# Kernel optimization log

Measured on AMD Instinct MI355X. Metric: run time of the kernel, lower is better.

Reference implementation:

```python
import jax, jax.numpy as jnp
import numpy as np

N_SAMPLES = 131072
N_FEATURES = 64
N_TREES = 64
DEPTH = 12                      # complete binary trees
N_INTERNAL = 2 ** DEPTH - 1     # 4095 internal nodes per tree
N_LEAVES = 2 ** DEPTH           # 4096 leaves per tree
N_CLASSES = 8


def setup_inputs() -> dict:
    key = jax.random.key(0)
    k1, k2, k3, k4 = jax.random.split(key, 4)
    X = jax.random.normal(k1, (N_SAMPLES, N_FEATURES), dtype=jnp.float32)
    # flattened complete-binary-tree parameters (FIL-style layout)
    features = jax.random.randint(k2, (N_TREES, N_INTERNAL), 0, N_FEATURES, dtype=jnp.int32)
    thresholds = jax.random.normal(k3, (N_TREES, N_INTERNAL), dtype=jnp.float32)
    leaf_values = jax.random.randint(k4, (N_TREES, N_LEAVES), 0, N_CLASSES, dtype=jnp.int32)
    return {"X": X, "features": features, "thresholds": thresholds, "leaf_values": leaf_values}


def reference(X, features, thresholds, leaf_values):
    # X: [N, F]; features/thresholds: [T, 2^D-1]; leaf_values: [T, 2^D]
    N = X.shape[0]
    row = jnp.arange(N)[None, :]                      # [1, N] broadcasts over trees
    node = jnp.zeros((N_TREES, N), dtype=jnp.int32)   # all samples start at root of every tree
    for _ in range(DEPTH):                            # fixed-depth traversal, fully vectorized
        f = jnp.take_along_axis(features, node, axis=1)      # [T, N] feature id per (tree, sample)
        t = jnp.take_along_axis(thresholds, node, axis=1)    # [T, N]
        xv = X[row, f]                                        # [T, N] gathered feature values
        node = 2 * node + 1 + (xv > t).astype(jnp.int32)      # go left (<=) or right (>)
    leaf_idx = node - N_INTERNAL                              # [T, N] in [0, 2^D)
    preds = jnp.take_along_axis(leaf_values, leaf_idx, axis=1)  # [T, N] per-tree class votes
    # majority vote == torch.mode over trees; argmax returns smallest class on ties,
    # matching torch.mode's smallest-modal-value convention
    counts = (preds[:, :, None] == jnp.arange(N_CLASSES)[None, None, :]).sum(axis=0)  # [N, C]
    return jnp.argmax(counts, axis=1)  # [N] final class predictions
```

## Files before the change

### kernel.cpp

```cpp
#include <hip/hip_runtime.h>


constexpr int kSamples  = 131072;
constexpr int kFeat     = 64;
constexpr int kTrees    = 64;
constexpr int kInternal = 4095;
constexpr int kClasses  = 8;

constexpr int TPB  = 512;
constexpr int XSTR = 512;
constexpr int XLDS_BYTES = kFeat * XSTR * 4;
constexpr int ILP  = 8;

struct Pair  { float thr0, thrL, thrR; unsigned meta; };
struct Sub16 { float thr10, thrL, thrR; unsigned meta; };

__global__ __launch_bounds__(256) void pack_pairs_kernel(
    const int* __restrict__ features, const float* __restrict__ thresholds,
    Pair* __restrict__ pairsA)
{
    int i = blockIdx.x * 256 + threadIdx.x;
    if (i >= kTrees * 341) return;
    int t = i / 341;
    int e = i - t * 341;
    int p, m;
    if      (e < 1)  { p = 0; m = e; }
    else if (e < 5)  { p = 1; m = e - 1; }
    else if (e < 21) { p = 2; m = e - 5; }
    else if (e < 85) { p = 3; m = e - 21; }
    else             { p = 4; m = e - 85; }
    int g0 = (1 << (2 * p)) - 1 + m;
    int b  = t * kInternal;
    int gL = 2 * g0 + 1, gR = 2 * g0 + 2;
    Pair pr;
    pr.thr0 = thresholds[b + g0];
    pr.thrL = thresholds[b + gL];
    pr.thrR = thresholds[b + gR];
    pr.meta = (unsigned)features[b + g0]
            | ((unsigned)features[b + gL] << 6)
            | ((unsigned)features[b + gR] << 12);
    pairsA[(t << 9) + e] = pr;
}

__global__ __launch_bounds__(256) void pack_sub_kernel(
    const int* __restrict__ features, const float* __restrict__ thresholds,
    const int* __restrict__ leaf_values, Sub16* __restrict__ subsA)
{
    int i = blockIdx.x * 256 + threadIdx.x;
    if (i >= kTrees * 1024) return;
    int t = i >> 10;
    int j = i & 1023;
    int n10 = 1023 + j;
    int b   = t * kInternal;
    int nL = 2 * n10 + 1, nR = 2 * n10 + 2;
    Sub16 sb;
    sb.thr10 = thresholds[b + n10];
    sb.thrL  = thresholds[b + nL];
    sb.thrR  = thresholds[b + nR];
    const int* lv = leaf_values + ((t << 12) + 4 * j);
    sb.meta = (unsigned)features[b + n10]
            | ((unsigned)features[b + nL] << 6)
            | ((unsigned)features[b + nR] << 12)
            | ((unsigned)lv[0] << 18) | ((unsigned)lv[1] << 21)
            | ((unsigned)lv[2] << 24) | ((unsigned)lv[3] << 27);
    subsA[(t << 10) + j] = sb;
}

__global__ __launch_bounds__(TPB, 2) void forest_kernel(
    const float* __restrict__ X,
    const Pair*  __restrict__ pairsA,
    const Sub16* __restrict__ subsA,
    int* __restrict__ out)
{
    extern __shared__ float xs[];
    const int tid  = threadIdx.x;
    const int base = blockIdx.x * TPB;

    {
        const float4* Xr = (const float4*)(X + (size_t)(base + tid) * kFeat);
        #pragma unroll
        for (int k = 0; k < kFeat / 4; ++k) {
            float4 v = Xr[k];
            xs[(4 * k + 0) * XSTR + tid] = v.x;
            xs[(4 * k + 1) * XSTR + tid] = v.y;
            xs[(4 * k + 2) * XSTR + tid] = v.z;
            xs[(4 * k + 3) * XSTR + tid] = v.w;
        }
    }
    __syncthreads();

    const char* xb = (const char*)xs + (tid << 2);
    unsigned long long votes = 0ull;

    const int mofs[5] = {0, 1, 5, 21, 85};

    for (int t0 = 0; t0 < kTrees; t0 += ILP) {
        int m[ILP];
        #pragma unroll
        for (int j = 0; j < ILP; ++j) m[j] = 0;

        #pragma unroll
        for (int p = 0; p < 5; ++p) {
            #pragma unroll
            for (int j = 0; j < ILP; ++j) {
                Pair pr = pairsA[((t0 + j) << 9) + mofs[p] + m[j]];
                float x0 = *(const float*)(xb + ((pr.meta & 63u) << 11));
                int c0 = x0 > pr.thr0 ? 1 : 0;
                float thr1     = c0 ? pr.thrR : pr.thrL;
                unsigned fsel  = c0 ? (pr.meta >> 12) : (pr.meta >> 6);
                float x1 = *(const float*)(xb + ((fsel & 63u) << 11));
                int c1 = x1 > thr1 ? 1 : 0;
                m[j] = 4 * m[j] + 2 * c0 + c1;
            }
        }

        #pragma unroll
        for (int j = 0; j < ILP; ++j) {
            Sub16 sb = subsA[((t0 + j) << 10) + m[j]];
            unsigned mt = sb.meta;
            float x0 = *(const float*)(xb + ((mt & 63u) << 11));
            int c0 = x0 > sb.thr10 ? 1 : 0;
            float thr1    = c0 ? sb.thrR : sb.thrL;
            unsigned fsel = c0 ? (mt >> 12) : (mt >> 6);
            float x1 = *(const float*)(xb + ((fsel & 63u) << 11));
            int c1 = x1 > thr1 ? 1 : 0;
            int cls = (mt >> (18 + 3 * ((c0 << 1) | c1))) & 7;
            votes += 1ull << (cls << 3);
        }
        __syncthreads();
    }

    int best = 0;
    int bc   = (int)(votes & 0xFFull);
    #pragma unroll
    for (int c = 1; c < kClasses; ++c) {
        int cnt = (int)((votes >> (c * 8)) & 0xFFull);
        if (cnt > bc) { bc = cnt; best = c; }
    }
    out[base + tid] = best;
}

extern "C" void kernel_launch(void* const* d_in, const int* in_sizes, int n_in,
                              void* d_out, int out_size, void* d_ws, size_t ws_size,
                              hipStream_t stream) {
    const float* X          = (const float*)d_in[0];
    const int*   features   = (const int*)d_in[1];
    const float* thresholds = (const float*)d_in[2];
    const int*   leaves     = (const int*)d_in[3];
    int*         out        = (int*)d_out;

    Pair*  pairsA = (Pair*)d_ws;
    Sub16* subsA  = (Sub16*)((char*)d_ws + (kTrees << 13));

    (void)hipFuncSetAttribute((const void*)forest_kernel,
                              hipFuncAttributeMaxDynamicSharedMemorySize,
                              XLDS_BYTES);

    pack_pairs_kernel<<<(kTrees * 341 + 255) / 256, 256, 0, stream>>>(
        features, thresholds, pairsA);
    pack_sub_kernel<<<(kTrees * 1024 + 255) / 256, 256, 0, stream>>>(
        features, thresholds, leaves, subsA);
    forest_kernel<<<kSamples / TPB, TPB, XLDS_BYTES, stream>>>(
        X, pairsA, subsA, out);
}
```

Before: 139.8 us.

## Stage level-8 tree pair nodes in LDS per tree group

For each group of eight trees, the block cooperatively copies the 256 level-8/9 pair nodes of each tree into shared memory. The fifth pair-level lookup then reads from LDS instead of doing a scattered global gather. This adds two barriers per tree group and raises LDS use from 128KB to 160KB per block, which cuts occupancy from two blocks per CU to one (launch bounds changed to match).

```diff
diff --git a/kernel.cpp b/kernel.cpp
--- a/kernel.cpp
+++ b/kernel.cpp
@@ -7,10 +7,12 @@
 constexpr int kInternal = 4095;
 constexpr int kClasses  = 8;
 
-constexpr int TPB  = 512;
-constexpr int XSTR = 512;
-constexpr int XLDS_BYTES = kFeat * XSTR * 4;
-constexpr int ILP  = 8;
+constexpr int TPB    = 512;
+constexpr int XSTR   = 512;
+constexpr int XBYTES = kFeat * XSTR * 4;
+constexpr int ILP    = 8;
+constexpr int P4N    = 256;
+constexpr int LDS_BYTES = XBYTES + ILP * P4N * 16;
 
 struct Pair  { float thr0, thrL, thrR; unsigned meta; };
 struct Sub16 { float thr10, thrL, thrR; unsigned meta; };
@@ -31,14 +33,13 @@
     else             { p = 4; m = e - 85; }
     int g0 = (1 << (2 * p)) - 1 + m;
     int b  = t * kInternal;
-    int gL = 2 * g0 + 1, gR = 2 * g0 + 2;
     Pair pr;
     pr.thr0 = thresholds[b + g0];
-    pr.thrL = thresholds[b + gL];
-    pr.thrR = thresholds[b + gR];
+    pr.thrL = thresholds[b + 2 * g0 + 1];
+    pr.thrR = thresholds[b + 2 * g0 + 2];
     pr.meta = (unsigned)features[b + g0]
-            | ((unsigned)features[b + gL] << 6)
-            | ((unsigned)features[b + gR] << 12);
+            | ((unsigned)features[b + 2 * g0 + 1] << 6)
+            | ((unsigned)features[b + 2 * g0 + 2] << 12);
     pairsA[(t << 9) + e] = pr;
 }
 
@@ -52,27 +53,29 @@
     int j = i & 1023;
     int n10 = 1023 + j;
     int b   = t * kInternal;
-    int nL = 2 * n10 + 1, nR = 2 * n10 + 2;
     Sub16 sb;
     sb.thr10 = thresholds[b + n10];
-    sb.thrL  = thresholds[b + nL];
-    sb.thrR  = thresholds[b + nR];
+    sb.thrL  = thresholds[b + 2 * n10 + 1];
+    sb.thrR  = thresholds[b + 2 * n10 + 2];
     const int* lv = leaf_values + ((t << 12) + 4 * j);
     sb.meta = (unsigned)features[b + n10]
-            | ((unsigned)features[b + nL] << 6)
-            | ((unsigned)features[b + nR] << 12)
+            | ((unsigned)features[b + 2 * n10 + 1] << 6)
+            | ((unsigned)features[b + 2 * n10 + 2] << 12)
             | ((unsigned)lv[0] << 18) | ((unsigned)lv[1] << 21)
             | ((unsigned)lv[2] << 24) | ((unsigned)lv[3] << 27);
     subsA[(t << 10) + j] = sb;
 }
 
-__global__ __launch_bounds__(TPB, 2) void forest_kernel(
+__global__ __launch_bounds__(TPB, 1) void forest_kernel(
     const float* __restrict__ X,
     const Pair*  __restrict__ pairsA,
     const Sub16* __restrict__ subsA,
     int* __restrict__ out)
 {
     extern __shared__ float xs[];
+    float4* __restrict__ p4buf = (float4*)((char*)xs + XBYTES);
+    const Pair* __restrict__ ldsP4 = (const Pair*)p4buf;
+
     const int tid  = threadIdx.x;
     const int base = blockIdx.x * TPB;
 
@@ -87,20 +90,32 @@
             xs[(4 * k + 3) * XSTR + tid] = v.w;
         }
     }
-    __syncthreads();
 
     const char* xb = (const char*)xs + (tid << 2);
     unsigned long long votes = 0ull;
 
-    const int mofs[5] = {0, 1, 5, 21, 85};
+    const int mofs[4] = {0, 1, 5, 21};
 
     for (int t0 = 0; t0 < kTrees; t0 += ILP) {
+        float4 pf[4];
+        #pragma unroll
+        for (int k = 0; k < 4; ++k) {
+            int idx = k * TPB + tid;
+            int j   = idx >> 8;
+            int m   = idx & 255;
+            pf[k] = ((const float4*)(pairsA + ((t0 + j) << 9) + 85))[m];
+        }
+        __syncthreads();
+        #pragma unroll
+        for (int k = 0; k < 4; ++k) p4buf[k * TPB + tid] = pf[k];
+        __syncthreads();
+
         int m[ILP];
         #pragma unroll
         for (int j = 0; j < ILP; ++j) m[j] = 0;
 
         #pragma unroll
-        for (int p = 0; p < 5; ++p) {
+        for (int p = 0; p < 4; ++p) {
             #pragma unroll
             for (int j = 0; j < ILP; ++j) {
                 Pair pr = pairsA[((t0 + j) << 9) + mofs[p] + m[j]];
@@ -116,6 +131,18 @@
 
         #pragma unroll
         for (int j = 0; j < ILP; ++j) {
+            Pair pr = ldsP4[(j << 8) + m[j]];
+            float x0 = *(const float*)(xb + ((pr.meta & 63u) << 11));
+            int c0 = x0 > pr.thr0 ? 1 : 0;
+            float thr1     = c0 ? pr.thrR : pr.thrL;
+            unsigned fsel  = c0 ? (pr.meta >> 12) : (pr.meta >> 6);
+            float x1 = *(const float*)(xb + ((fsel & 63u) << 11));
+            int c1 = x1 > thr1 ? 1 : 0;
+            m[j] = 4 * m[j] + 2 * c0 + c1;
+        }
+
+        #pragma unroll
+        for (int j = 0; j < ILP; ++j) {
             Sub16 sb = subsA[((t0 + j) << 10) + m[j]];
             unsigned mt = sb.meta;
             float x0 = *(const float*)(xb + ((mt & 63u) << 11));
@@ -127,7 +154,6 @@
             int cls = (mt >> (18 + 3 * ((c0 << 1) | c1))) & 7;
             votes += 1ull << (cls << 3);
         }
-        __syncthreads();
     }
 
     int best = 0;
@@ -154,12 +180,12 @@
 
     (void)hipFuncSetAttribute((const void*)forest_kernel,
                               hipFuncAttributeMaxDynamicSharedMemorySize,
-                              XLDS_BYTES);
+                              LDS_BYTES);
 
     pack_pairs_kernel<<<(kTrees * 341 + 255) / 256, 256, 0, stream>>>(
         features, thresholds, pairsA);
     pack_sub_kernel<<<(kTrees * 1024 + 255) / 256, 256, 0, stream>>>(
         features, thresholds, leaves, subsA);
-    forest_kernel<<<kSamples / TPB, TPB, XLDS_BYTES, stream>>>(
+    forest_kernel<<<kSamples / TPB, TPB, LDS_BYTES, stream>>>(
         X, pairsA, subsA, out);
 }
```

Measured after the change: 150.4 us. +7.6%, slower.
